# Optimization experiments

Hardware: AMD Instinct MI355X
Metric: run time of the kernel (lower is better)

Reference implementation:

```python
import jax, jax.numpy as jnp
import numpy as np
from jax import lax

# SLAYER neuron / simulation constants (from netParams yaml)
THETA = 1.0      # spike threshold
TS = 1.0         # simulation time step
TAU_SR = 10.0    # PSP (SRM) kernel time constant
TAU_REF = 1.0    # refractory kernel time constant
SCALE_REF = 2.0  # refractory kernel scale (x theta)
TAU_RHO = 1.0    # surrogate-gradient pdf width
SCALE_RHO = 1.0  # surrogate-gradient pdf scale
T_BINS = 2048    # nTimeBins = tSample / Ts
K_SRM = 100      # truncated SRM kernel length
K_REF = 32       # truncated refractory kernel length


def _srm_kernel():
    t = jnp.arange(K_SRM, dtype=jnp.float32) * TS
    return (t / TAU_SR) * jnp.exp(1.0 - t / TAU_SR)


def _ref_tail():
    # refractory response added to membrane at times t+1 .. t+K_REF after a spike
    t = jnp.arange(K_REF, dtype=jnp.float32) * TS
    ref = -SCALE_REF * THETA * (t / TAU_REF) * jnp.exp(1.0 - t / TAU_REF)
    return jnp.concatenate([ref[1:], jnp.zeros((1,), jnp.float32)])


SRM = _srm_kernel()
REF_TAIL = _ref_tail()


def psp(x):
    # causal temporal FIR along last axis: out[t] = sum_k SRM[k] * x[t-k]
    sh = x.shape
    xf = x.reshape(-1, 1, sh[-1])
    w = jnp.flip(SRM).reshape(1, 1, K_SRM).astype(x.dtype)
    y = lax.conv_general_dilated(xf, w, (1,), [(K_SRM - 1, 0)],
                                 dimension_numbers=('NCH', 'OIH', 'NCH'))
    return y.reshape(sh)


def _spike_scan(p):
    # p: [..., T]; sequential threshold + refractory dynamics over time
    pT = jnp.moveaxis(p, -1, 0)
    buf0 = jnp.zeros(p.shape[:-1] + (K_REF,), p.dtype)
    ref = REF_TAIL.astype(p.dtype)

    def step(buf, pt):
        u = pt + buf[..., 0]                      # membrane potential
        s = (u >= THETA).astype(p.dtype) / TS     # hard threshold spike
        buf = jnp.concatenate([buf[..., 1:], jnp.zeros_like(buf[..., :1])], -1) \
              + s[..., None] * ref
        return buf, (s, u)

    _, (sT, uT) = lax.scan(step, buf0, pT)
    return jnp.moveaxis(sT, 0, -1), jnp.moveaxis(uT, 0, -1)


@jax.custom_vjp
def spike(p):
    return _spike_scan(p)[0]


def _spike_fwd(p):
    s, u = _spike_scan(p)
    return s, u


def _spike_bwd(u, g):
    # SLAYER surrogate gradient: pdf of spike escape noise around threshold
    pdf = (SCALE_RHO / TAU_RHO) * jnp.exp(-jnp.abs(u - THETA) / TAU_RHO)
    return (g * pdf,)


spike.defvjp(_spike_fwd, _spike_bwd)


def conv2d_t(x, w):
    # x: [1,C,H,W,T]; same 2D 'VALID' conv applied at every time step
    xt = jnp.moveaxis(x[0], -1, 0)  # [T,C,H,W]
    y = lax.conv_general_dilated(xt, w, (1, 1), 'VALID',
                                 dimension_numbers=('NCHW', 'OIHW', 'NCHW'))
    return jnp.moveaxis(y, 0, -1)[None]


def pool_t(x):
    # SLAYER pool: per-channel 2x2 sum with constant weight 1.1*theta, stride 2
    _, C, H, W, T = x.shape
    xt = jnp.moveaxis(x[0], -1, 0).reshape(T * C, 1, H, W)
    w = jnp.full((1, 1, 2, 2), 1.1 * THETA, x.dtype)
    y = lax.conv_general_dilated(xt, w, (2, 2), 'VALID',
                                 dimension_numbers=('NCHW', 'OIHW', 'NCHW'))
    y = y.reshape(T, C, H // 2, W // 2)
    return jnp.moveaxis(y, 0, -1)[None]


def dense_t(x, w):
    # x: [1,Cin,1,1,T], w: [Cout,Cin] -> [1,Cout,1,1,T]
    return jnp.einsum('nchwt,oc->nohwt', x, w)


def forward(x, Wc1, Wc2, Wf1, Wf2, Wf3):
    # replicate(input, nTimeBins): nearest-interp == broadcast along new time axis
    xr = jnp.broadcast_to(x[..., None], x.shape + (T_BINS,)).reshape(1, 3, 32, 32, T_BINS)
    h = spike(psp(conv2d_t(xr, Wc1)))   # [1,6,28,28,T]
    h = spike(psp(pool_t(h)))           # [1,6,14,14,T]
    h = spike(psp(conv2d_t(h, Wc2)))    # [1,16,10,10,T]
    h = h.reshape(1, 16 * 10 * 10, 1, 1, T_BINS)
    h = spike(psp(dense_t(h, Wf1)))     # [1,300,1,1,T]
    h = spike(psp(dense_t(h, Wf2)))     # [1,150,1,1,T]
    h = spike(psp(dense_t(h, Wf3)))     # [1,10,1,1,T]
    return h


def setup_inputs() -> dict:
    key = jax.random.key(0)
    ks = jax.random.split(key, 6)
    x = jax.random.uniform(ks[0], (1, 3, 32, 32), jnp.float32)
    Wc1 = jax.random.normal(ks[1], (6, 3, 5, 5), jnp.float32) * 0.15
    Wc2 = jax.random.normal(ks[2], (16, 6, 5, 5), jnp.float32) * 0.08
    Wf1 = jax.random.normal(ks[3], (300, 1600), jnp.float32) * 0.03
    Wf2 = jax.random.normal(ks[4], (150, 300), jnp.float32) * 0.07
    Wf3 = jax.random.normal(ks[5], (10, 150), jnp.float32) * 0.1
    return {"x": x, "Wc1": Wc1, "Wc2": Wc2, "Wf1": Wf1, "Wf2": Wf2, "Wf3": Wf3}


def reference(x, Wc1, Wc2, Wf1, Wf2, Wf3):
    return forward(x, Wc1, Wc2, Wf1, Wf2, Wf3)
```

## Files before the change

### kernel.cpp

```cpp
#include <hip/hip_runtime.h>
#include <math.h>


#define T_BINS 2048
#define K_SRM  100
#define AEXP   0.36787944117144233
#define CHK    32
#define WUP    48
#define NCHK   (T_BINS / CHK)
#define FIXS   35184372088832.0
#define KSP    56

typedef __attribute__((ext_vector_type(8))) short          s16x8;
typedef __attribute__((ext_vector_type(8))) unsigned short u16x8;
typedef __attribute__((ext_vector_type(4))) float          f32x4;

__global__ __launch_bounds__(256) void k_prep(
    const float* __restrict__ x, const float* __restrict__ Wc1,
    const float* __restrict__ Wf1, const float* __restrict__ Wf2,
    const float* __restrict__ Wf3, float* __restrict__ c1,
    double* __restrict__ Scum, double* __restrict__ H,
    float* __restrict__ WT2, float* __restrict__ WT3,
    unsigned short* __restrict__ BL) {
  int b = blockIdx.x, tid = threadIdx.x;
  if (b < 19) {
    int idx = b * 256 + tid;
    if (idx >= 4704) return;
    int o = idx / 784, r = idx % 784, i = r / 28, j = r % 28;
    double acc = 0.0;
    for (int ci = 0; ci < 3; ++ci)
      for (int ky = 0; ky < 5; ++ky) {
        const float* xr = x + ci * 1024 + (i + ky) * 32 + j;
        const float* wr = Wc1 + ((o * 3 + ci) * 5 + ky) * 5;
#pragma unroll
        for (int kx = 0; kx < 5; ++kx)
          acc += (double)xr[kx] * (double)wr[kx];
      }
    c1[idx] = (float)acc;
  } else if (b < 299) {
    int idx = (b - 19) * 256 + tid;
    if (idx >= KSP * 320 * 4) return;
    int g = idx & 3, rest = idx >> 2;
    int n = rest % 320, ks = rest / 320;
    u16x8 out[6];
#pragma unroll
    for (int j = 0; j < 6; ++j)
#pragma unroll
      for (int jj = 0; jj < 8; ++jj) out[j][jj] = 0;
    if (n < 300 && ks < 50) {
      const float* wr = Wf1 + (size_t)n * 1600 + ks * 32 + g * 8;
#pragma unroll
      for (int jj = 0; jj < 8; ++jj) {
        long long v = llrint((double)wr[jj] * FIXS);
#pragma unroll
        for (int j = 0; j < 6; ++j) {
          int d = (int)(signed char)(v & 0xFF);
          v = (v - d) >> 8;
          float fd = (float)d;
          unsigned int fb = __float_as_uint(fd);
          out[j][jj] = (unsigned short)(fb >> 16);
        }
      }
    }
#pragma unroll
    for (int j = 0; j < 6; ++j)
      ((u16x8*)BL)[((j * KSP + ks) * 320 + n) * 4 + g] = out[j];
  } else if (b < 481) {
    int idx = (b - 299) * 256 + tid;
    if (idx < 45000) {
      int c = idx / 150, o = idx - c * 150;
      WT2[idx] = Wf2[o * 300 + c];
    } else if (idx < 46500) {
      int j = idx - 45000, c = j / 10, o = j - c * 10;
      WT3[j] = Wf3[o * 150 + c];
    }
  } else {
    if (tid == 0) {
      double acc = 0.0;
      for (int k = 0; k < K_SRM; ++k) {
        double tk = (double)k;
        double h = (tk * 0.1) * exp(1.0 - tk * 0.1);
        H[k] = h; acc += h; Scum[k] = acc;
      }
      H[100] = 0.0; H[101] = 0.0;
    }
  }
}

__global__ __launch_bounds__(256) void k_scan1_chunk(
    const float* __restrict__ c1, const double* __restrict__ Scum_g,
    unsigned char* __restrict__ s1b) {
  __shared__ double Sc[K_SRM];
  for (int k = threadIdx.x; k < K_SRM; k += 256) Sc[k] = Scum_g[k];
  __syncthreads();
  int idx = blockIdx.x * 256 + threadIdx.x;
  int chunk = idx / 4704, n = idx - chunk * 4704;
  int t0 = chunk * CHK;
  int ts = t0 - WUP; if (ts < 0) ts = 0;
  double w = (double)c1[n];
  double e1 = 0.0, e2 = 0.0;
  double u = w * Sc[ts < (K_SRM - 1) ? ts : (K_SRM - 1)];
  unsigned char* outp = s1b + n;
  for (int t = ts; t < t0; ++t) {
    double s = (u >= 1.0) ? 1.0 : 0.0;
    int si = t + 1 < (K_SRM - 1) ? t + 1 : (K_SRM - 1);
    u = w * Sc[si] - 2.0 * ((e1 + e2) + s);
    double t1 = e1 + s;
    e2 = AEXP * (e2 + t1); e1 = AEXP * t1;
  }
#pragma unroll 8
  for (int t = t0; t < t0 + CHK; ++t) {
    double s = (u >= 1.0) ? 1.0 : 0.0;
    outp[(size_t)t * 4704] = (unsigned char)s;
    int si = t + 1 < (K_SRM - 1) ? t + 1 : (K_SRM - 1);
    u = w * Sc[si] - 2.0 * ((e1 + e2) + s);
    double t1 = e1 + s;
    e2 = AEXP * (e2 + t1); e1 = AEXP * t1;
  }
}

__global__ __launch_bounds__(256) void k_pool(const unsigned char* __restrict__ s1b,
                                              unsigned char* __restrict__ y2b) {
  int idx = blockIdx.x * blockDim.x + threadIdx.x;
  if (idx >= 1176 * T_BINS) return;
  int t = idx / 1176, n2 = idx - t * 1176;
  int c = n2 / 196, r = n2 % 196, i = r / 14, j = r % 14;
  const unsigned char* b = s1b + (size_t)t * 4704 + c * 784 + (2 * i) * 28 + 2 * j;
  y2b[idx] = (unsigned char)((int)b[0] + (int)b[1] + (int)b[28] + (int)b[29]);
}

template <typename Tin, typename Tout>
__global__ __launch_bounds__(256) void k_psp_scan_chunk(
    const Tin* __restrict__ z, Tout* __restrict__ sout, int N,
    long strideT, long strideN, const double* __restrict__ H_g,
    double A1, double A2, double B1, double C0, double C1, double xscale) {
  __shared__ double Hs[102];
  for (int k = threadIdx.x; k < 102; k += 256) Hs[k] = H_g[k];
  __syncthreads();
  int idx = blockIdx.x * blockDim.x + threadIdx.x;
  if (idx >= NCHK * N) return;
  int chunk = idx / N, n = idx - chunk * N;
  int t0 = chunk * CHK;
  int ts = t0 - WUP; if (ts < 0) ts = 0;
  const Tin* zn = z + n;

  double accA = 0.0, accB = 0.0;
  float fA[10], fB[10];
#define LOADF(BUF, J0)                                               \
  { _Pragma("unroll")                                                \
    for (int q_ = 0; q_ < 10; ++q_)                                  \
      BUF[q_] = (float)zn[(long)(ts - 1 - ((J0) + q_)) * (long)N]; }
#define FMA10(BUF, J0)                                               \
  { _Pragma("unroll")                                                \
    for (int q_ = 0; q_ < 10; ++q_) {                                \
      double v_ = (double)BUF[q_];                                   \
      accA += Hs[(J0) + q_ + 1] * v_;                                \
      accB += Hs[(J0) + q_] * v_;                                    \
    } }
  LOADF(fA, 0)
  for (int q = 0; q < 100; q += 20) {
    LOADF(fB, q + 10)
    FMA10(fA, q)
    LOADF(fA, q + 20)
    FMA10(fB, q + 10)
  }
#undef LOADF
#undef FMA10
  double pp1 = accA * xscale;
  double pp2 = accB * xscale;
  double xm100 = (double)(float)zn[(long)(ts - 100) * (long)N];
  double u = pp1, e1 = 0.0, e2 = 0.0;

  float cA[8], cB[8], lA[8], lB[8];
  size_t oa = (size_t)n * (size_t)strideN + (size_t)t0 * (size_t)strideT;
  int nwg = (t0 - ts) >> 3;
  int ngrp = nwg + CHK / 8;
#define PREF8(CBUF, LBUF, TB)                                        \
  { long tb_ = (long)(TB);                                           \
    _Pragma("unroll")                                                \
    for (int j_ = 0; j_ < 8; ++j_) {                                 \
      CBUF[j_] = (float)zn[(tb_ + j_) * (long)N];                    \
      LBUF[j_] = (float)zn[(tb_ + j_ - 99) * (long)N];               \
    } }
#define PROC8(CBUF, LBUF, DOSTORE)                                   \
  { _Pragma("unroll")                                                \
    for (int j_ = 0; j_ < 8; ++j_) {                                 \
      double s = (u >= 1.0) ? 1.0 : 0.0;                             \
      if (DOSTORE) { sout[oa] = (Tout)s; oa += (size_t)strideT; }    \
      double xt = (double)CBUF[j_], x99 = (double)LBUF[j_];          \
      double pn = A1 * pp1 - A2 * pp2 + B1 * xt - C0 * x99           \
                  + C1 * xm100;                                      \
      xm100 = x99;                                                   \
      u = pn - 2.0 * ((e1 + e2) + s);                                \
      double t1 = e1 + s;                                            \
      e2 = AEXP * (e2 + t1); e1 = AEXP * t1;                         \
      pp2 = pp1; pp1 = pn;                                           \
    } }
  PREF8(cA, lA, ts)
  for (int g = 0; g < ngrp; g += 2) {
    PREF8(cB, lB, ts + (g + 1) * 8)
    PROC8(cA, lA, g >= nwg)
    PREF8(cA, lA, ts + (g + 2) * 8)
    PROC8(cB, lB, g + 1 >= nwg)
  }
#undef PREF8
#undef PROC8
}

__global__ __launch_bounds__(192) void k_conv2(const unsigned char* __restrict__ s2b,
                                               const float* __restrict__ W,
                                               float* __restrict__ z3) {
  __shared__ float ls[1176];
  __shared__ float lw[2400];
  int t = blockIdx.x;
  for (int i = threadIdx.x; i < 1176; i += 192)
    ls[i] = (float)s2b[(size_t)t * 1176 + i];
  for (int i = threadIdx.x; i < 2400; i += 192) lw[i] = W[i];
  __syncthreads();
  int tid = threadIdx.x;
  if (tid >= 160) return;
  int o = tid / 10, i = tid - o * 10;
  double acc[10];
#pragma unroll
  for (int j = 0; j < 10; ++j) acc[j] = 0.0;
  for (int ci = 0; ci < 6; ++ci)
#pragma unroll
    for (int ky = 0; ky < 5; ++ky) {
      const float* lr = &ls[ci * 196 + (i + ky) * 14];
      const float* wr = &lw[((o * 6 + ci) * 5 + ky) * 5];
      double r[14], w[5];
#pragma unroll
      for (int q = 0; q < 14; ++q) r[q] = (double)lr[q];
#pragma unroll
      for (int q = 0; q < 5; ++q) w[q] = (double)wr[q];
#pragma unroll
      for (int j = 0; j < 10; ++j)
        acc[j] += r[j] * w[0] + r[j + 1] * w[1] + r[j + 2] * w[2] +
                  r[j + 3] * w[3] + r[j + 4] * w[4];
    }
  float* zr = z3 + (size_t)t * 1600 + o * 100 + i * 10;
#pragma unroll
  for (int j = 0; j < 10; ++j) zr[j] = (float)acc[j];
}

__global__ __launch_bounds__(512, 2) void k_mfma_dense1(
    const unsigned char* __restrict__ s3b, const unsigned short* __restrict__ BL,
    float* __restrict__ z4) {
  __shared__ float redf[8][64][41];
  int bid = blockIdx.x;
  int xcd = bid & 7;
  int ct = xcd & 3;
  int bm = (bid >> 3) | ((xcd >> 2) << 5);
  int col0 = ct * 80;
  int w = threadIdx.x >> 6, lane = threadIdx.x & 63;
  int r = lane & 15, g = lane >> 4;
  int ks0 = w * 7;
  int rowA = bm * 32 + r, rowB = rowA + 16;
  const unsigned char* abA = s3b + (size_t)rowA * 1600 + ks0 * 32 + g * 8;
  const unsigned char* abB = s3b + (size_t)rowB * 1600 + ks0 * 32 + g * 8;

  s16x8 aA[7], aB[7];
#pragma unroll
  for (int ks = 0; ks < 7; ++ks) {
    unsigned long long bA = *(const unsigned long long*)(abA + ks * 32);
    unsigned long long bB = *(const unsigned long long*)(abB + ks * 32);
    u16x8 fa, fb;
#pragma unroll
    for (int jj = 0; jj < 8; ++jj) {
      fa[jj] = ((bA >> (8 * jj)) & 1ULL) ? (unsigned short)0x3F80
                                         : (unsigned short)0;
      fb[jj] = ((bB >> (8 * jj)) & 1ULL) ? (unsigned short)0x3F80
                                         : (unsigned short)0;
    }
    aA[ks] = (s16x8)fa; aB[ks] = (s16x8)fb;
  }

  double zawA[4] = {0.0, 0.0, 0.0, 0.0};
  double zawB[4] = {0.0, 0.0, 0.0, 0.0};
  double scale = 1.0;
  for (int j = 0; j < 6; ++j) {
    f32x4 CA[5], CB[5];
#pragma unroll
    for (int nt = 0; nt < 5; ++nt) {
      CA[nt] = (f32x4){0.f, 0.f, 0.f, 0.f};
      CB[nt] = (f32x4){0.f, 0.f, 0.f, 0.f};
    }
#pragma unroll
    for (int ks = 0; ks < 7; ++ks) {
      const u16x8* bb =
          (const u16x8*)BL + ((size_t)((j * KSP + ks0 + ks) * 320 + col0 + r)) * 4 + g;
#pragma unroll
      for (int nt = 0; nt < 5; ++nt) {
        s16x8 bf = (s16x8)bb[nt * 64];
        CA[nt] = __builtin_amdgcn_mfma_f32_16x16x32_bf16(aA[ks], bf, CA[nt], 0, 0, 0);
        CB[nt] = __builtin_amdgcn_mfma_f32_16x16x32_bf16(aB[ks], bf, CB[nt], 0, 0, 0);
      }
    }
#pragma unroll
    for (int nt = 0; nt < 5; ++nt)
#pragma unroll
      for (int q = 0; q < 4; ++q) {
        redf[w][lane][nt * 4 + q]      = CA[nt][q];
        redf[w][lane][20 + nt * 4 + q] = CB[nt][q];
      }
    __syncthreads();
    if (w < 5) {
#pragma unroll
      for (int q = 0; q < 4; ++q) {
        int i = w * 4 + q;
        float sA = ((redf[0][lane][i] + redf[1][lane][i]) +
                    (redf[2][lane][i] + redf[3][lane][i])) +
                   ((redf[4][lane][i] + redf[5][lane][i]) +
                    (redf[6][lane][i] + redf[7][lane][i]));
        int i2 = 20 + i;
        float sB = ((redf[0][lane][i2] + redf[1][lane][i2]) +
                    (redf[2][lane][i2] + redf[3][lane][i2])) +
                   ((redf[4][lane][i2] + redf[5][lane][i2]) +
                    (redf[6][lane][i2] + redf[7][lane][i2]));
        zawA[q] += scale * (double)sA;
        zawB[q] += scale * (double)sB;
      }
    }
    __syncthreads();
    scale *= 256.0;
  }

  if (w < 5) {
    int col = col0 + w * 16 + r;
    if (col < 300) {
      int rA0 = bm * 32 + g * 4, rB0 = rA0 + 16;
#pragma unroll
      for (int q = 0; q < 4; ++q) {
        z4[(size_t)(rA0 + q) * 300 + col] = (float)(zawA[q] * (1.0 / FIXS));
        z4[(size_t)(rB0 + q) * 300 + col] = (float)(zawB[q] * (1.0 / FIXS));
      }
    }
  }
}

template <int NIN, int NOUT, int BLK>
__global__ __launch_bounds__(BLK) void k_dense_sparse(
    const unsigned char* __restrict__ s, const float* __restrict__ WT,
    float* __restrict__ z) {
  constexpr int NCH = (NIN + BLK - 1) / BLK;
  constexpr int NW = BLK / 64;
  __shared__ __align__(16) int list[NIN];
  __shared__ int wcnt[NCH][NW];
  int t = blockIdx.x;
  const unsigned char* srow = s + (size_t)t * NIN;
  int tid = threadIdx.x, lane = tid & 63, wv = tid >> 6;
  unsigned long long msave[NCH];
  bool asave[NCH];
#pragma unroll
  for (int ci = 0; ci < NCH; ++ci) {
    int c = ci * BLK + tid;
    bool a = (c < NIN) && (srow[c] != 0);
    unsigned long long m = __ballot(a);
    msave[ci] = m; asave[ci] = a;
    if (lane == 0) wcnt[ci][wv] = __popcll(m);
  }
  __syncthreads();
  int nact = 0;
#pragma unroll
  for (int ci = 0; ci < NCH; ++ci) {
    int off = nact;
    for (int w = 0; w < wv; ++w) off += wcnt[ci][w];
    if (asave[ci])
      list[off + __popcll(msave[ci] & ((1ULL << lane) - 1))] = ci * BLK + tid;
    for (int w = 0; w < NW; ++w) nact += wcnt[ci][w];
  }
  __syncthreads();
  if (tid >= NOUT) return;
  const float* col = WT + tid;
  double a0 = 0.0, a1 = 0.0, a2 = 0.0, a3 = 0.0;
  int k = 0, nact4 = nact & ~3;
  for (; k < nact4; k += 4) {
    int4 l4 = *(const int4*)&list[k];
    a0 += (double)col[(size_t)l4.x * NOUT];
    a1 += (double)col[(size_t)l4.y * NOUT];
    a2 += (double)col[(size_t)l4.z * NOUT];
    a3 += (double)col[(size_t)l4.w * NOUT];
  }
  for (; k < nact; ++k) a0 += (double)col[(size_t)list[k] * NOUT];
  z[(size_t)t * NOUT + tid] = (float)((a0 + a1) + (a2 + a3));
}

extern "C" void kernel_launch(void* const* d_in, const int* in_sizes, int n_in,
                              void* d_out, int out_size, void* d_ws, size_t ws_size,
                              hipStream_t stream) {
  const float* x   = (const float*)d_in[0];
  const float* Wc1 = (const float*)d_in[1];
  const float* Wc2 = (const float*)d_in[2];
  const float* Wf1 = (const float*)d_in[3];
  const float* Wf2 = (const float*)d_in[4];
  const float* Wf3 = (const float*)d_in[5];
  float* out = (float*)d_out;
  char* ws = (char*)d_ws;

  double* Scum = (double*)(ws + 0);
  double* Htab = (double*)(ws + 2048);
  float*  c1   = (float*)(ws + 4096);
  const size_t PADZ = 65536;
  const size_t ZA   = PADZ + 655360;
  const size_t PADY = ZA + 13107200 + 262144;
  const size_t Y2B  = PADY + 131072;
  const size_t S1B  = Y2B + 2408448 + 65536;
  const size_t S2B  = S1B + 9633792;
  const size_t S3B  = S2B + 2408448;
  const size_t S4B  = S3B + 3276800;
  const size_t S5B  = S4B + 614400;
  const size_t WB   = S5B + 307200;
  const size_t WC   = WB + 180000;
  const size_t BLa  = 33122000;
  float* zA = (float*)(ws + ZA);
  unsigned char* y2b = (unsigned char*)(ws + Y2B);
  unsigned char* s1b = (unsigned char*)(ws + S1B);
  unsigned char* s2b = (unsigned char*)(ws + S2B);
  unsigned char* s3b = (unsigned char*)(ws + S3B);
  unsigned char* s4b = (unsigned char*)(ws + S4B);
  unsigned char* s5b = (unsigned char*)(ws + S5B);
  float* WT2 = (float*)(ws + WB);
  float* WT3 = (float*)(ws + WC);
  unsigned short* BLp = (unsigned short*)(ws + BLa);

  double b = exp(-0.1), c = 0.1 * exp(1.0);
  double A1 = 2.0 * b, A2 = b * b;
  double B1 = c * b;
  double C0 = 100.0 * c * pow(b, 100.0);
  double C1 = 99.0 * c * pow(b, 101.0);
  double sc = (double)1.1f;

  hipMemsetAsync(ws + PADZ, 0, 655360, stream);
  hipMemsetAsync(ws + PADY, 0, 131072, stream);
  k_prep<<<482, 256, 0, stream>>>(x, Wc1, Wf1, Wf2, Wf3, c1, Scum, Htab,
                                  WT2, WT3, BLp);
  k_scan1_chunk<<<NCHK * 4704 / 256, 256, 0, stream>>>(c1, Scum, s1b);
  k_pool<<<(1176 * T_BINS) / 256, 256, 0, stream>>>(s1b, y2b);
  k_psp_scan_chunk<unsigned char, unsigned char>
      <<<(NCHK * 1176 + 255) / 256, 256, 0, stream>>>(
      y2b, s2b, 1176, 1176L, 1L, Htab, A1, A2, B1 * sc, C0 * sc, C1 * sc, sc);
  k_conv2<<<T_BINS, 192, 0, stream>>>(s2b, Wc2, zA);
  k_psp_scan_chunk<float, unsigned char>
      <<<(NCHK * 1600 + 255) / 256, 256, 0, stream>>>(
      zA, s3b, 1600, 1600L, 1L, Htab, A1, A2, B1, C0, C1, 1.0);
  k_mfma_dense1<<<256, 512, 0, stream>>>(s3b, BLp, zA);
  k_psp_scan_chunk<float, unsigned char>
      <<<(NCHK * 300 + 255) / 256, 256, 0, stream>>>(
      zA, s4b, 300, 300L, 1L, Htab, A1, A2, B1, C0, C1, 1.0);
  k_dense_sparse<300, 150, 192><<<T_BINS, 192, 0, stream>>>(s4b, WT2, zA);
  k_psp_scan_chunk<float, unsigned char>
      <<<(NCHK * 150 + 255) / 256, 256, 0, stream>>>(
      zA, s5b, 150, 150L, 1L, Htab, A1, A2, B1, C0, C1, 1.0);
  k_dense_sparse<150, 10, 64><<<T_BINS, 64, 0, stream>>>(s5b, WT3, zA);
  k_psp_scan_chunk<float, float>
      <<<(NCHK * 10 + 255) / 256, 256, 0, stream>>>(
      zA, out, 10, 1L, 2048L, Htab, A1, A2, B1, C0, C1, 1.0);

  (void)in_sizes; (void)n_in; (void)out_size; (void)ws_size;
}
```

Before: 217.7 us.

## Rewrite conv2 as im2col bf16 MFMA with fixed-point split weights

Replaces the scalar double-precision conv2 kernel with an MFMA kernel. Binary spike inputs are gathered im2col-style into bf16 A fragments, and the weights are pre-split in the prep kernel into six signed 8-bit fixed-point digits stored as bf16, so the products stay exact. Each wave handles one time step and accumulates the digit partial sums in double with power-of-256 scaling, which removes the heavy FP64 FMA work. It adds a prep stage, a gather from LDS per fragment element, and six MFMA passes per tile.

```diff
diff --git a/kernel.cpp b/kernel.cpp
--- a/kernel.cpp
+++ b/kernel.cpp
@@ -17,11 +17,11 @@
 
 __global__ __launch_bounds__(256) void k_prep(
     const float* __restrict__ x, const float* __restrict__ Wc1,
-    const float* __restrict__ Wf1, const float* __restrict__ Wf2,
-    const float* __restrict__ Wf3, float* __restrict__ c1,
-    double* __restrict__ Scum, double* __restrict__ H,
+    const float* __restrict__ Wc2, const float* __restrict__ Wf1,
+    const float* __restrict__ Wf2, const float* __restrict__ Wf3,
+    float* __restrict__ c1, double* __restrict__ Scum, double* __restrict__ H,
     float* __restrict__ WT2, float* __restrict__ WT3,
-    unsigned short* __restrict__ BL) {
+    unsigned short* __restrict__ BL, unsigned short* __restrict__ BL2) {
   int b = blockIdx.x, tid = threadIdx.x;
   if (b < 19) {
     int idx = b * 256 + tid;
@@ -74,6 +74,34 @@
       int j = idx - 45000, c = j / 10, o = j - c * 10;
       WT3[j] = Wf3[o * 150 + c];
     }
+  } else if (b < 483) {
+    int idx = (b - 481) * 256 + tid;
+    if (idx >= 320) return;
+    int g = idx & 3, rest = idx >> 2;
+    int o = rest & 15, ks = rest >> 4;
+    u16x8 out[6];
+#pragma unroll
+    for (int j = 0; j < 6; ++j)
+#pragma unroll
+      for (int jj = 0; jj < 8; ++jj) out[j][jj] = 0;
+#pragma unroll
+    for (int jj = 0; jj < 8; ++jj) {
+      int k = ks * 32 + g * 8 + jj;
+      if (k < 150) {
+        long long v = llrint((double)Wc2[o * 150 + k] * FIXS);
+#pragma unroll
+        for (int j = 0; j < 6; ++j) {
+          int d = (int)(signed char)(v & 0xFF);
+          v = (v - d) >> 8;
+          float fd = (float)d;
+          unsigned int fb = __float_as_uint(fd);
+          out[j][jj] = (unsigned short)(fb >> 16);
+        }
+      }
+    }
+#pragma unroll
+    for (int j = 0; j < 6; ++j)
+      ((u16x8*)BL2)[((j * 5 + ks) * 4 + g) * 16 + o] = out[j];
   } else {
     if (tid == 0) {
       double acc = 0.0;
@@ -207,40 +235,69 @@
 #undef PROC8
 }
 
-__global__ __launch_bounds__(192) void k_conv2(const unsigned char* __restrict__ s2b,
-                                               const float* __restrict__ W,
-                                               float* __restrict__ z3) {
-  __shared__ float ls[1176];
-  __shared__ float lw[2400];
-  int t = blockIdx.x;
-  for (int i = threadIdx.x; i < 1176; i += 192)
-    ls[i] = (float)s2b[(size_t)t * 1176 + i];
-  for (int i = threadIdx.x; i < 2400; i += 192) lw[i] = W[i];
+__global__ __launch_bounds__(256, 2) void k_conv2_mfma(
+    const unsigned char* __restrict__ s2b, const unsigned short* __restrict__ BL2g,
+    float* __restrict__ z3) {
+  __shared__ __align__(16) unsigned short bl2[15360];
+  __shared__ unsigned char ls[4][1216];
+  __shared__ int tab[160];
+  int tid = threadIdx.x;
+  for (int i = tid; i < 7680; i += 256)
+    ((unsigned int*)bl2)[i] = ((const unsigned int*)BL2g)[i];
+  if (tid < 160) {
+    int k = tid;
+    int ci = k / 25, rem = k - ci * 25;
+    int ky = rem / 5, kx = rem - ky * 5;
+    tab[k] = (k < 150) ? (ci * 196 + ky * 14 + kx) : 0;
+  }
+  int w = tid >> 6, lane = tid & 63;
+  int t = blockIdx.x * 4 + w;
+  {
+    const unsigned int* srow = (const unsigned int*)(s2b + (size_t)t * 1176);
+    unsigned int* dst = (unsigned int*)ls[w];
+    for (int i = lane; i < 294; i += 64) dst[i] = srow[i];
+  }
   __syncthreads();
-  int tid = threadIdx.x;
-  if (tid >= 160) return;
-  int o = tid / 10, i = tid - o * 10;
-  double acc[10];
-#pragma unroll
-  for (int j = 0; j < 10; ++j) acc[j] = 0.0;
-  for (int ci = 0; ci < 6; ++ci)
-#pragma unroll
-    for (int ky = 0; ky < 5; ++ky) {
-      const float* lr = &ls[ci * 196 + (i + ky) * 14];
-      const float* wr = &lw[((o * 6 + ci) * 5 + ky) * 5];
-      double r[14], w[5];
-#pragma unroll
-      for (int q = 0; q < 14; ++q) r[q] = (double)lr[q];
-#pragma unroll
-      for (int q = 0; q < 5; ++q) w[q] = (double)wr[q];
-#pragma unroll
-      for (int j = 0; j < 10; ++j)
-        acc[j] += r[j] * w[0] + r[j + 1] * w[1] + r[j + 2] * w[2] +
-                  r[j + 3] * w[3] + r[j + 4] * w[4];
-    }
-  float* zr = z3 + (size_t)t * 1600 + o * 100 + i * 10;
-#pragma unroll
-  for (int j = 0; j < 10; ++j) zr[j] = (float)acc[j];
+  int r = lane & 15, g = lane >> 4;
+#pragma unroll
+  for (int mt = 0; mt < 7; ++mt) {
+    int p = mt * 16 + r;
+    int pi = p / 10;
+    int pioff = pi * 14 + (p - pi * 10);
+    s16x8 a[5];
+#pragma unroll
+    for (int ks = 0; ks < 5; ++ks) {
+      u16x8 f;
+#pragma unroll
+      for (int jj = 0; jj < 8; ++jj) {
+        int k = ks * 32 + g * 8 + jj;
+        bool v = (mt < 6 || p < 100) && (ks < 4 || k < 150);
+        int idx = v ? (tab[k] + pioff) : 0;
+        unsigned char byte = ls[w][idx];
+        f[jj] = (v && byte) ? (unsigned short)0x3F80 : (unsigned short)0;
+      }
+      a[ks] = (s16x8)f;
+    }
+    double zacc[4] = {0.0, 0.0, 0.0, 0.0};
+    double scale = 1.0;
+    for (int j = 0; j < 6; ++j) {
+      f32x4 C = (f32x4){0.f, 0.f, 0.f, 0.f};
+#pragma unroll
+      for (int ks = 0; ks < 5; ++ks) {
+        const u16x8* bf = (const u16x8*)bl2 + (((j * 5 + ks) * 4 + g) * 16 + r);
+        C = __builtin_amdgcn_mfma_f32_16x16x32_bf16(a[ks], (s16x8)(*bf), C, 0, 0, 0);
+      }
+#pragma unroll
+      for (int q = 0; q < 4; ++q) zacc[q] += scale * (double)C[q];
+      scale *= 256.0;
+    }
+#pragma unroll
+    for (int q = 0; q < 4; ++q) {
+      int pr = mt * 16 + g * 4 + q;
+      if (pr < 100)
+        z3[(size_t)t * 1600 + r * 100 + pr] = (float)(zacc[q] * (1.0 / FIXS));
+    }
+  }
 }
 
 __global__ __launch_bounds__(512, 2) void k_mfma_dense1(
@@ -412,6 +469,7 @@
   const size_t WB   = S5B + 307200;
   const size_t WC   = WB + 180000;
   const size_t BLa  = 33122000;
+  const size_t BL2a = BLa + 6881280;
   float* zA = (float*)(ws + ZA);
   unsigned char* y2b = (unsigned char*)(ws + Y2B);
   unsigned char* s1b = (unsigned char*)(ws + S1B);
@@ -421,7 +479,8 @@
   unsigned char* s5b = (unsigned char*)(ws + S5B);
   float* WT2 = (float*)(ws + WB);
   float* WT3 = (float*)(ws + WC);
-  unsigned short* BLp = (unsigned short*)(ws + BLa);
+  unsigned short* BLp  = (unsigned short*)(ws + BLa);
+  unsigned short* BL2p = (unsigned short*)(ws + BL2a);
 
   double b = exp(-0.1), c = 0.1 * exp(1.0);
   double A1 = 2.0 * b, A2 = b * b;
@@ -432,14 +491,14 @@
 
   hipMemsetAsync(ws + PADZ, 0, 655360, stream);
   hipMemsetAsync(ws + PADY, 0, 131072, stream);
-  k_prep<<<482, 256, 0, stream>>>(x, Wc1, Wf1, Wf2, Wf3, c1, Scum, Htab,
-                                  WT2, WT3, BLp);
+  k_prep<<<484, 256, 0, stream>>>(x, Wc1, Wc2, Wf1, Wf2, Wf3, c1, Scum, Htab,
+                                  WT2, WT3, BLp, BL2p);
   k_scan1_chunk<<<NCHK * 4704 / 256, 256, 0, stream>>>(c1, Scum, s1b);
   k_pool<<<(1176 * T_BINS) / 256, 256, 0, stream>>>(s1b, y2b);
   k_psp_scan_chunk<unsigned char, unsigned char>
       <<<(NCHK * 1176 + 255) / 256, 256, 0, stream>>>(
       y2b, s2b, 1176, 1176L, 1L, Htab, A1, A2, B1 * sc, C0 * sc, C1 * sc, sc);
-  k_conv2<<<T_BINS, 192, 0, stream>>>(s2b, Wc2, zA);
+  k_conv2_mfma<<<T_BINS / 4, 256, 0, stream>>>(s2b, BL2p, zA);
   k_psp_scan_chunk<float, unsigned char>
       <<<(NCHK * 1600 + 255) / 256, 256, 0, stream>>>(
       zA, s3b, 1600, 1600L, 1L, Htab, A1, A2, B1, C0, C1, 1.0);
```

Result: faster. 198.8 us, median of 3 (-8.7%).
